# Kernel tuning notes

Hardware: AMD Instinct MI355X
Metric: run time of the kernel (lower is better)

Reference implementation:

```python
import jax, jax.numpy as jnp
import numpy as np

CAP = 15.0
EPS = 1e-6
NUM_HEADS = 16
HEAD_DIM = 64

def _rmsnorm(x, w):
    xf = x.astype(jnp.float32)
    var = jnp.mean(xf * xf, axis=-1, keepdims=True)
    return w * (xf * jax.lax.rsqrt(var + EPS)).astype(x.dtype)

def _gate(g):
    # sigmoid(soft_cap(g)) with cap 15
    return jax.nn.sigmoid(CAP * jnp.tanh(g / CAP))

def setup_inputs() -> dict:
    key = jax.random.key(0)
    ks = jax.random.split(key, 4)
    B, S, D = 4, 2048, 1024
    H, Dh = NUM_HEADS, HEAD_DIM
    return {
        "x": jax.random.normal(ks[0], (B, S, D), jnp.float32),
        "hidden_state": jnp.zeros((B, H, Dh, Dh), jnp.float32),
        "w_rms": jnp.ones((D,), jnp.float32),
        "w_qkv": jax.random.normal(ks[1], (D, 3 * H * Dh), jnp.float32) * 0.02,
        "w_gate": jax.random.normal(ks[2], (D, 3 * H), jnp.float32) * 0.02,
        "w_out": jax.random.normal(ks[3], (D, D), jnp.float32) * 0.02,
    }

def reference(x, hidden_state, w_rms, w_qkv, w_gate, w_out):
    B, S, D = x.shape
    H, Dh = NUM_HEADS, HEAD_DIM
    residual = x
    xn = _rmsnorm(x, w_rms)
    qkv = (xn @ w_qkv).reshape(B, S, 3, H, Dh)
    q, k, v = qkv[:, :, 0], qkv[:, :, 1], qkv[:, :, 2]  # [B,S,H,Dh]
    gates = _gate((xn @ w_gate).reshape(B, S, 3, H))
    i_g, f_g, o_g = gates[:, :, 0], gates[:, :, 1], gates[:, :, 2]  # [B,S,H]

    # time-major for scan: [S,B,H,...]
    def tm(a):
        return jnp.moveaxis(a, 1, 0)

    def step(state, inp):
        qt, kt, vt, it, ft, ot = inp  # [B,H,Dh]/[B,H]
        kv = kt[..., :, None] * vt[..., None, :]            # [B,H,Dh,Dh]
        state = ft[..., None, None] * state + it[..., None, None] * kv
        h = jnp.einsum('bhd,bhde->bhe', qt, state) * ot[..., None]
        return state, h

    _, h_seq = jax.lax.scan(step, hidden_state,
                            (tm(q), tm(k), tm(v), tm(i_g), tm(f_g), tm(o_g)))
    out = jnp.moveaxis(h_seq, 0, 1).reshape(B, S, H * Dh) @ w_out
    return residual + out
```

## Files before the change

### kernel.cpp

```cpp
#include <hip/hip_runtime.h>
#include <math.h>

typedef unsigned short u16;
typedef unsigned int   u32;
typedef __bf16 bf16x8 __attribute__((ext_vector_type(8)));
typedef float  f32x4  __attribute__((ext_vector_type(4)));

#define NBATCH 4
#define SEQ    2048
#define DIM    1024
#define NH     16
#define BH     64
#define NC     32
#define ROWS   8192
#define N1     3328

__device__ __forceinline__ u16 f2bf(float f) {
  u32 u = __builtin_bit_cast(u32, f);
  u32 r = u + 0x7fffu + ((u >> 16) & 1u);
  return (u16)(r >> 16);
}
__device__ __forceinline__ float bf2f(u16 h) {
  return __builtin_bit_cast(float, (u32)h << 16);
}

__device__ __forceinline__ void gl2lds16(const u16* g, u16* l) {
  __builtin_amdgcn_global_load_lds(
      (const __attribute__((address_space(1))) u32*)g,
      (__attribute__((address_space(3))) u32*)l, 16, 0, 0);
}

__global__ __launch_bounds__(256) void transpose_w(const float* __restrict__ W,
                                                   u16* __restrict__ Bt, int K, int N) {
  __shared__ float tile[32][33];
  const int n0 = blockIdx.x * 32, k0 = blockIdx.y * 32;
  const int tx = threadIdx.x, ty = threadIdx.y;
  #pragma unroll
  for (int i = 0; i < 4; i++)
    tile[ty + i * 8][tx] = W[(size_t)(k0 + ty + i * 8) * N + n0 + tx];
  __syncthreads();
  #pragma unroll
  for (int i = 0; i < 4; i++)
    Bt[(size_t)(n0 + ty + i * 8) * K + k0 + tx] = f2bf(tile[tx][ty + i * 8]);
}

__global__ __launch_bounds__(256) void fill_gateW(const float* __restrict__ wg,
                                                  u16* __restrict__ Bt) {
  const int g = blockIdx.x;
  const int tid = threadIdx.x;
  #pragma unroll
  for (int kk = 0; kk < 4; kk++) {
    const int k = kk * 256 + tid;
    u16 v = 0;
    if (g < 48) v = f2bf(wg[(size_t)k * 48 + g]);
    Bt[(size_t)(3072 + g) * 1024 + k] = v;
  }
}

__global__ __launch_bounds__(256) void rmsnorm_k(const float* __restrict__ x,
                                                 const float* __restrict__ w,
                                                 u16* __restrict__ xn) {
  const int row = blockIdx.x, tid = threadIdx.x;
  const float4 xv = *(const float4*)&x[(size_t)row * 1024 + tid * 4];
  float ss = xv.x * xv.x + xv.y * xv.y + xv.z * xv.z + xv.w * xv.w;
  #pragma unroll
  for (int off = 32; off > 0; off >>= 1) ss += __shfl_down(ss, off);
  __shared__ float red[4];
  if ((tid & 63) == 0) red[tid >> 6] = ss;
  __syncthreads();
  const float tot = red[0] + red[1] + red[2] + red[3];
  const float scale = rsqrtf(tot * (1.0f / 1024.0f) + 1e-6f);
  const float4 wv = *(const float4*)&w[tid * 4];
  const u16 o0 = f2bf(xv.x * scale * wv.x), o1 = f2bf(xv.y * scale * wv.y);
  const u16 o2 = f2bf(xv.z * scale * wv.z), o3 = f2bf(xv.w * scale * wv.w);
  uint2 ov;
  ov.x = (u32)o0 | ((u32)o1 << 16);
  ov.y = (u32)o2 | ((u32)o3 << 16);
  *(uint2*)&xn[(size_t)row * 1024 + tid * 4] = ov;
}


#define FENCE asm volatile("" ::: "memory")
#define SBAR  do { FENCE; __builtin_amdgcn_s_barrier(); FENCE; } while (0)
#define WAITV4 do { FENCE; asm volatile("s_waitcnt vmcnt(4)" ::: "memory"); } while (0)
#define WAITV0 do { FENCE; asm volatile("s_waitcnt vmcnt(0)" ::: "memory"); } while (0)

#define STAGE_A(BUF, HALF, TILE) do { \
  const u16* s_ = Abase + (size_t)(TILE) * 64 + (size_t)(HALF) * 131072; \
  u16* l_ = &lds[((BUF) * 4 + (HALF)) * 8192 + tid * 8]; \
  gl2lds16(s_, l_); gl2lds16(s_ + 65536, l_ + 4096); \
} while (0)

#define STAGE_B(BUF, HALF, TILE) do { \
  const u16* s_ = Bbase + (size_t)(TILE) * 64 + (size_t)(HALF) * 131072; \
  u16* l_ = &lds[((BUF) * 4 + 2 + (HALF)) * 8192 + tid * 8]; \
  gl2lds16(s_, l_); gl2lds16(s_ + 65536, l_ + 4096); \
} while (0)

#define READ_A(ALDS, MH) do { \
  _Pragma("unroll") \
  for (int mi_ = 0; mi_ < 4; ++mi_) { \
    af[mi_][0] = *(const bf16x8*)((ALDS) + (MH) * 4096 + mi_ * 1024 + co0); \
    af[mi_][1] = *(const bf16x8*)((ALDS) + (MH) * 4096 + mi_ * 1024 + co1); \
  } \
} while (0)

#define READ_B(BLDS, NH) do { \
  _Pragma("unroll") \
  for (int ni_ = 0; ni_ < 2; ++ni_) { \
    bfr[NH][ni_][0] = *(const bf16x8*)((BLDS) + (NH) * 2048 + ni_ * 1024 + co0); \
    bfr[NH][ni_][1] = *(const bf16x8*)((BLDS) + (NH) * 2048 + ni_ * 1024 + co1); \
  } \
} while (0)

#define MFMA16(MH, NH) do { \
  __builtin_amdgcn_s_setprio(1); \
  _Pragma("unroll") \
  for (int mi_ = 0; mi_ < 4; ++mi_) { \
    _Pragma("unroll") \
    for (int ni_ = 0; ni_ < 2; ++ni_) { \
      acc[(MH)*4+mi_][(NH)*2+ni_] = __builtin_amdgcn_mfma_f32_16x16x32_bf16( \
          af[mi_][0], bfr[NH][ni_][0], acc[(MH)*4+mi_][(NH)*2+ni_], 0, 0, 0); \
      acc[(MH)*4+mi_][(NH)*2+ni_] = __builtin_amdgcn_mfma_f32_16x16x32_bf16( \
          af[mi_][1], bfr[NH][ni_][1], acc[(MH)*4+mi_][(NH)*2+ni_], 0, 0, 0); \
    } \
  } \
  __builtin_amdgcn_s_setprio(0); \
} while (0)

#define GITER(T, FULL) do { \
   READ_A(aLds0, 0); READ_B(bLds0, 0); STAGE_A(1, 0, 2*(T)+1); \
         SBAR; MFMA16(0, 0); SBAR; \
   READ_B(bLds0, 1); STAGE_A(1, 1, 2*(T)+1); \
         SBAR; MFMA16(0, 1); SBAR; \
   READ_A(aLds0, 1); if (FULL) STAGE_B(0, 0, 2*(T)+2); \
         SBAR; MFMA16(1, 0); SBAR; \
   if (FULL) STAGE_B(0, 1, 2*(T)+2); \
         SBAR; MFMA16(1, 1); if (FULL) { WAITV4; } else { WAITV0; } SBAR; \
   READ_A(aLds1, 0); READ_B(bLds1, 0); if (FULL) STAGE_A(0, 0, 2*(T)+2); \
         SBAR; MFMA16(0, 0); SBAR; \
   READ_B(bLds1, 1); if (FULL) STAGE_A(0, 1, 2*(T)+2); \
         SBAR; MFMA16(0, 1); SBAR; \
   READ_A(aLds1, 1); if (FULL) STAGE_B(1, 0, 2*(T)+3); \
         SBAR; MFMA16(1, 0); SBAR; \
   if (FULL) STAGE_B(1, 1, 2*(T)+3); \
         SBAR; MFMA16(1, 1); if (FULL) { WAITV4; } SBAR; \
} while (0)

#define CORE_SETUP(AROWBASE, BCOLBASE) \
  const int tid = threadIdx.x; \
  const int lane = tid & 63, wave = tid >> 6; \
  const int q = lane >> 4, m16 = lane & 15; \
  const int wm = wave & 1, wn = wave >> 1; \
  const int sx = m16 & 7; \
  const int co0 = (q ^ sx) * 8; \
  const int co1 = ((4 + q) ^ sx) * 8; \
  const int r0 = tid >> 3, pc = tid & 7; \
  const int lcg = pc ^ (r0 & 7); \
  const u16* Abase = (AROWBASE) + (size_t)r0 * 1024 + lcg * 8; \
  const u16* Bbase = (BCOLBASE) + (size_t)r0 * 1024 + lcg * 8; \
  const u16* aLds0 = &lds[wm * 8192 + m16 * 64]; \
  const u16* aLds1 = aLds0 + 32768; \
  const u16* bLds0 = &lds[16384 + (wn >> 1) * 8192 + ((wn & 1) * 64 + m16) * 64]; \
  const u16* bLds1 = bLds0 + 32768; \
  bf16x8 af[4][2]; \
  bf16x8 bfr[2][2][2]; \
  f32x4 acc[8][4] = {};

#define CORE_RUN16() do { \
  STAGE_A(0, 0, 0); STAGE_A(0, 1, 0); STAGE_B(0, 0, 0); STAGE_B(0, 1, 0); \
  STAGE_B(1, 0, 1); STAGE_B(1, 1, 1); \
  WAITV4; SBAR; \
  _Pragma("unroll 1") \
  for (int t = 0; t < 7; ++t) GITER(t, 1); \
  GITER(7, 0); \
} while (0)

__global__ __launch_bounds__(512, 2) void gemm_qkv(const u16* __restrict__ A, const u16* __restrict__ Bt,
                                                   u16* __restrict__ Qb, u16* __restrict__ Kb,
                                                   u16* __restrict__ Vb, float* __restrict__ gates) {
  __shared__ __attribute__((aligned(16))) u16 lds[65536];

  const int g = blockIdx.x;
  const int swz = (g & 7) * 52 + (g >> 3);
  const int bm = swz / 13, bn = swz % 13;
  const int rowBase = bm * 256, colBase = bn * 256;

  CORE_SETUP(A + (size_t)rowBase * 1024, Bt + (size_t)colBase * 1024);
  CORE_RUN16();

  const int rr = lane >> 2, co = (lane & 3) * 16;
  if (colBase < 3072) {
    const int which = colBase >> 10;
    u16* dstBase = (which == 0) ? Qb : ((which == 1) ? Kb : Vb);
    const int b = rowBase >> 11;
    const int h = ((colBase & 1023) >> 6) + wn;
    const int tRow0 = (rowBase & 2047) + wm * 128;
    u16* headBase = dstBase + ((size_t)(b * 16 + h)) * 2048 * 64;
    u16* scratch = lds + wave * 1024;
    #pragma unroll
    for (int mi = 0; mi < 8; ++mi) {
      #pragma unroll
      for (int bj = 0; bj < 4; ++bj)
        #pragma unroll
        for (int r = 0; r < 4; ++r)
          scratch[(q * 4 + r) * 64 + bj * 16 + m16] = f2bf(acc[mi][bj][r]);
      const uint4 d0 = *(const uint4*)&scratch[rr * 64 + co];
      const uint4 d1 = *(const uint4*)&scratch[rr * 64 + co + 8];
      u16* gp = headBase + (size_t)(tRow0 + mi * 16 + rr) * 64 + co;
      *(uint4*)gp = d0;
      *(uint4*)(gp + 8) = d1;
    }
  } else {
    if (wn == 0) {
      #pragma unroll
      for (int ai = 0; ai < 8; ++ai)
        #pragma unroll
        for (int bj = 0; bj < 3; ++bj)
          #pragma unroll
          for (int r = 0; r < 4; ++r) {
            const int grow = rowBase + wm * 128 + ai * 16 + q * 4 + r;
            const int b = grow >> 11, tt = grow & 2047;
            const float v = acc[ai][bj][r];
            const float gg = 1.0f / (1.0f + expf(-(15.0f * tanhf(v * (1.0f / 15.0f)))));
            gates[((size_t)bj * 64 + (b * 16 + m16)) * 2048 + tt] = gg;
          }
    }
  }
}

__global__ __launch_bounds__(512, 2) void gemm_out(const u16* __restrict__ A, const u16* __restrict__ Bt,
                                                   const float* __restrict__ resid,
                                                   float* __restrict__ out) {
  __shared__ __attribute__((aligned(16))) u16 lds[65536];

  const int g = blockIdx.x;
  const int swz = (g & 7) * 16 + (g >> 3);
  const int bm = swz >> 2, bn = swz & 3;
  const int rowBase = bm * 256, colBase = bn * 256;

  CORE_SETUP(A + (size_t)rowBase * 1024, Bt + (size_t)colBase * 1024);
  CORE_RUN16();

  const int colW = colBase + (wn >> 1) * 128 + (wn & 1) * 64;
  #pragma unroll
  for (int mi = 0; mi < 8; ++mi)
    #pragma unroll
    for (int bj = 0; bj < 4; ++bj)
      #pragma unroll
      for (int r = 0; r < 4; ++r) {
        const int grow = rowBase + wm * 128 + mi * 16 + q * 4 + r;
        const int gcol = colW + bj * 16 + m16;
        const size_t idx = (size_t)grow * 1024 + gcol;
        out[idx] = acc[mi][bj][r] + resid[idx];
      }
}

__global__ __launch_bounds__(256) void passA_k(const u16* __restrict__ Qb, const u16* __restrict__ Kb,
                                               const u16* __restrict__ Vb,
                                               const float* __restrict__ gates,
                                               float* __restrict__ la,
                                               u16* __restrict__ Mbuf, u16* __restrict__ hseq) {
  __shared__ u16 Ql[64][72], Kl[64][72], KTl[64][72], VTl[64][72], Pl[64][72];
  __shared__ float laS[64], iS[64];
  const int tid = threadIdx.x;
  const int bh = blockIdx.x >> 5, c = blockIdx.x & 31;
  const int lane = tid & 63, w = tid >> 6;
  const int q = lane >> 4, m16 = lane & 15;
  const size_t base = ((size_t)bh * 2048 + c * 64) * 64;
  const int toff = c * 64;

  if (tid < 64) {
    float lg = logf(gates[(size_t)(64 + bh) * 2048 + toff + tid]);
    #pragma unroll
    for (int off = 1; off < 64; off <<= 1) {
      const float y = __shfl_up(lg, off);
      if (tid >= off) lg += y;
    }
    laS[tid] = lg;
    iS[tid] = gates[(size_t)bh * 2048 + toff + tid];
    la[(size_t)bh * 2048 + toff + tid] = lg;
  }
  __syncthreads();

  {
    const int s = tid >> 2, db = (tid & 3) * 16;
    const float wk = expf(laS[63] - laS[s]) * iS[s];
    const uint4 q0 = *(const uint4*)&Qb[base + s * 64 + db];
    const uint4 q1 = *(const uint4*)&Qb[base + s * 64 + db + 8];
    *(uint4*)&Ql[s][db] = q0;
    *(uint4*)&Ql[s][db + 8] = q1;
    const uint4 k0 = *(const uint4*)&Kb[base + s * 64 + db];
    const uint4 k1 = *(const uint4*)&Kb[base + s * 64 + db + 8];
    *(uint4*)&Kl[s][db] = k0;
    *(uint4*)&Kl[s][db + 8] = k1;
    u16 ktmp[16];
    *(uint4*)&ktmp[0] = k0;
    *(uint4*)&ktmp[8] = k1;
    #pragma unroll
    for (int j = 0; j < 16; j++) KTl[db + j][s] = f2bf(wk * bf2f(ktmp[j]));
    const uint4 v0 = *(const uint4*)&Vb[base + s * 64 + db];
    const uint4 v1 = *(const uint4*)&Vb[base + s * 64 + db + 8];
    u16 vtmp[16];
    *(uint4*)&vtmp[0] = v0;
    *(uint4*)&vtmp[8] = v1;
    #pragma unroll
    for (int j = 0; j < 16; j++) VTl[db + j][s] = vtmp[j];
  }
  __syncthreads();

  f32x4 pacc[4] = {};
  #pragma unroll
  for (int ks = 0; ks < 2; ks++) {
    const bf16x8 aq = *(const bf16x8*)&Ql[w * 16 + m16][ks * 32 + q * 8];
    #pragma unroll
    for (int ni = 0; ni < 4; ni++) {
      const bf16x8 bk = *(const bf16x8*)&Kl[ni * 16 + m16][ks * 32 + q * 8];
      pacc[ni] = __builtin_amdgcn_mfma_f32_16x16x32_bf16(aq, bk, pacc[ni], 0, 0, 0);
    }
  }
  #pragma unroll
  for (int ni = 0; ni < 4; ni++)
    #pragma unroll
    for (int r = 0; r < 4; r++) {
      const int tt = w * 16 + q * 4 + r, ss = ni * 16 + m16;
      float Wts = 0.0f;
      if (ss <= tt) Wts = expf(laS[tt] - laS[ss]) * iS[ss];
      Pl[tt][ss] = f2bf(pacc[ni][r] * Wts);
    }
  __syncthreads();

  f32x4 hacc[4] = {}, macc[4] = {};
  #pragma unroll
  for (int ks = 0; ks < 2; ks++) {
    const bf16x8 ap = *(const bf16x8*)&Pl[w * 16 + m16][ks * 32 + q * 8];
    const bf16x8 av = *(const bf16x8*)&VTl[w * 16 + m16][ks * 32 + q * 8];
    #pragma unroll
    for (int ni = 0; ni < 4; ni++) {
      const bf16x8 bv = *(const bf16x8*)&VTl[ni * 16 + m16][ks * 32 + q * 8];
      const bf16x8 bk = *(const bf16x8*)&KTl[ni * 16 + m16][ks * 32 + q * 8];
      hacc[ni] = __builtin_amdgcn_mfma_f32_16x16x32_bf16(ap, bv, hacc[ni], 0, 0, 0);
      macc[ni] = __builtin_amdgcn_mfma_f32_16x16x32_bf16(av, bk, macc[ni], 0, 0, 0);
    }
  }
  const int b = bh >> 4, h = bh & 15;
  #pragma unroll
  for (int ni = 0; ni < 4; ni++)
    #pragma unroll
    for (int r = 0; r < 4; r++) {
      const int tt = w * 16 + q * 4 + r, e = ni * 16 + m16;
      const int tg = c * 64 + tt;
      hseq[((size_t)b * 2048 + tg) * 1024 + h * 64 + e] = f2bf(hacc[ni][r]);
      Mbuf[(((size_t)bh * 32 + c) * 64 + tt) * 64 + e] = f2bf(macc[ni][r]);
    }
}

__global__ __launch_bounds__(256) void passB_k(u16* __restrict__ Mbuf,
                                               const float* __restrict__ hidden,
                                               const float* __restrict__ la) {
  const int bh = blockIdx.x >> 4;
  const int e = (blockIdx.x & 15) * 256 + threadIdx.x;
  __shared__ float Gs[32];
  if (threadIdx.x < 32)
    Gs[threadIdx.x] = expf(la[(size_t)bh * 2048 + threadIdx.x * 64 + 63]);
  __syncthreads();
  const int eRow = e >> 6, dCol = e & 63;
  float st = hidden[(size_t)bh * 4096 + dCol * 64 + eRow];
  u16* M = &Mbuf[(size_t)bh * 32 * 4096 + e];
  float m_next = bf2f(M[0]);
  #pragma unroll 4
  for (int c = 0; c < 32; c++) {
    const float m_cur = m_next;
    if (c < 31) m_next = bf2f(M[(size_t)(c + 1) * 4096]);
    M[(size_t)c * 4096] = f2bf(st);
    st = Gs[c] * st + m_cur;
  }
}

__global__ __launch_bounds__(256) void passC_k(const u16* __restrict__ Qb,
                                               const u16* __restrict__ SprevT,
                                               const float* __restrict__ la,
                                               const float* __restrict__ gates,
                                               u16* __restrict__ hseq) {
  __shared__ u16 aQl[64][72], STl[64][72];
  __shared__ float laS[64], oS[64];
  const int tid = threadIdx.x;
  const int bh = blockIdx.x >> 5, c = blockIdx.x & 31;
  const int lane = tid & 63, w = tid >> 6;
  const int q = lane >> 4, m16 = lane & 15;
  const size_t base = ((size_t)bh * 2048 + c * 64) * 64;
  const int toff = c * 64;
  if (tid < 64) {
    laS[tid] = la[(size_t)bh * 2048 + toff + tid];
    oS[tid] = gates[(size_t)(128 + bh) * 2048 + toff + tid];
  }
  {
    const int s = tid >> 2, db = (tid & 3) * 16;
    *(uint4*)&aQl[s][db]     = *(const uint4*)&Qb[base + s * 64 + db];
    *(uint4*)&aQl[s][db + 8] = *(const uint4*)&Qb[base + s * 64 + db + 8];
    const u16* SpT = &SprevT[((size_t)bh * 32 + c) * 4096];
    *(uint4*)&STl[s][db]     = *(const uint4*)&SpT[s * 64 + db];
    *(uint4*)&STl[s][db + 8] = *(const uint4*)&SpT[s * 64 + db + 8];
  }
  __syncthreads();
  f32x4 acc[4] = {};
  #pragma unroll
  for (int ks = 0; ks < 2; ks++) {
    const bf16x8 a = *(const bf16x8*)&aQl[w * 16 + m16][ks * 32 + q * 8];
    #pragma unroll
    for (int ni = 0; ni < 4; ni++) {
      const bf16x8 bb = *(const bf16x8*)&STl[ni * 16 + m16][ks * 32 + q * 8];
      acc[ni] = __builtin_amdgcn_mfma_f32_16x16x32_bf16(a, bb, acc[ni], 0, 0, 0);
    }
  }
  const int b = bh >> 4, h = bh & 15;
  #pragma unroll
  for (int ni = 0; ni < 4; ni++)
    #pragma unroll
    for (int r = 0; r < 4; r++) {
      const int tt = w * 16 + q * 4 + r, e = ni * 16 + m16;
      const int tg = c * 64 + tt;
      const float a_t = expf(laS[tt]);
      const float o = oS[tt];
      const size_t idx = ((size_t)b * 2048 + tg) * 1024 + h * 64 + e;
      hseq[idx] = f2bf(o * (bf2f(hseq[idx]) + a_t * acc[ni][r]));
    }
}

extern "C" void kernel_launch(void* const* d_in, const int* in_sizes, int n_in,
                              void* d_out, int out_size, void* d_ws, size_t ws_size,
                              hipStream_t stream) {
  (void)in_sizes; (void)n_in; (void)out_size; (void)ws_size;
  const float* x      = (const float*)d_in[0];
  const float* hidden = (const float*)d_in[1];
  const float* w_rms  = (const float*)d_in[2];
  const float* w_qkv  = (const float*)d_in[3];
  const float* w_gate = (const float*)d_in[4];
  const float* w_out  = (const float*)d_in[5];
  float* out = (float*)d_out;

  char* p = (char*)d_ws;
  u16* wqkvT = (u16*)p;  p += (size_t)N1 * 1024 * 2;
  u16* woutT = (u16*)p;  p += (size_t)1024 * 1024 * 2;
  u16* xn    = (u16*)p;  p += (size_t)ROWS * 1024 * 2;
  u16* Qb    = (u16*)p;  p += (size_t)BH * 2048 * 64 * 2;
  u16* Kb    = (u16*)p;  p += (size_t)BH * 2048 * 64 * 2;
  u16* Vb    = (u16*)p;  p += (size_t)BH * 2048 * 64 * 2;
  float* gates = (float*)p; p += (size_t)3 * BH * 2048 * 4;
  float* la    = (float*)p; p += (size_t)BH * 2048 * 4;
  u16* Mbuf  = (u16*)p;  p += (size_t)BH * NC * 4096 * 2;
  u16* hseq  = (u16*)p;  p += (size_t)ROWS * 1024 * 2;

  transpose_w<<<dim3(96, 32), dim3(32, 8), 0, stream>>>(w_qkv, wqkvT, 1024, 3072);
  transpose_w<<<dim3(32, 32), dim3(32, 8), 0, stream>>>(w_out, woutT, 1024, 1024);
  fill_gateW<<<256, 256, 0, stream>>>(w_gate, wqkvT);
  rmsnorm_k<<<ROWS, 256, 0, stream>>>(x, w_rms, xn);
  gemm_qkv<<<416, 512, 0, stream>>>(xn, wqkvT, Qb, Kb, Vb, gates);
  passA_k<<<BH * NC, 256, 0, stream>>>(Qb, Kb, Vb, gates, la, Mbuf, hseq);
  passB_k<<<BH * 16, 256, 0, stream>>>(Mbuf, hidden, la);
  passC_k<<<BH * NC, 256, 0, stream>>>(Qb, Mbuf, la, gates, hseq);
  gemm_out<<<128, 512, 0, stream>>>(hseq, woutT, x, out);
}
```

Measured before the change: 258.6 us.

## Stage chunk outputs through LDS for vector stores, use fast math, reswizzle GEMM tiles

passA and passC now stage their MFMA results in shared memory and write hseq and Mbuf as 16-byte vector stores per row, replacing scattered 2-byte global writes. This is meant to cut uncoalesced global store and read-modify-write traffic. Both GEMMs switch their block-to-tile mapping so consecutive swizzled blocks walk rows first. expf and logf become the __expf and __logf intrinsics, trading a little accuracy in the gates and decay weights for fewer instructions.

```diff
diff --git a/kernel.cpp b/kernel.cpp
--- a/kernel.cpp
+++ b/kernel.cpp
@@ -183,7 +183,7 @@
 
   const int g = blockIdx.x;
   const int swz = (g & 7) * 52 + (g >> 3);
-  const int bm = swz / 13, bn = swz % 13;
+  const int bm = swz & 31, bn = swz >> 5;
   const int rowBase = bm * 256, colBase = bn * 256;
 
   CORE_SETUP(A + (size_t)rowBase * 1024, Bt + (size_t)colBase * 1024);
@@ -222,7 +222,7 @@
             const int grow = rowBase + wm * 128 + ai * 16 + q * 4 + r;
             const int b = grow >> 11, tt = grow & 2047;
             const float v = acc[ai][bj][r];
-            const float gg = 1.0f / (1.0f + expf(-(15.0f * tanhf(v * (1.0f / 15.0f)))));
+            const float gg = 1.0f / (1.0f + __expf(-(15.0f * tanhf(v * (1.0f / 15.0f)))));
             gates[((size_t)bj * 64 + (b * 16 + m16)) * 2048 + tt] = gg;
           }
     }
@@ -236,7 +236,7 @@
 
   const int g = blockIdx.x;
   const int swz = (g & 7) * 16 + (g >> 3);
-  const int bm = swz >> 2, bn = swz & 3;
+  const int bm = swz & 31, bn = swz >> 5;
   const int rowBase = bm * 256, colBase = bn * 256;
 
   CORE_SETUP(A + (size_t)rowBase * 1024, Bt + (size_t)colBase * 1024);
@@ -271,7 +271,7 @@
   const int toff = c * 64;
 
   if (tid < 64) {
-    float lg = logf(gates[(size_t)(64 + bh) * 2048 + toff + tid]);
+    float lg = __logf(gates[(size_t)(64 + bh) * 2048 + toff + tid]);
     #pragma unroll
     for (int off = 1; off < 64; off <<= 1) {
       const float y = __shfl_up(lg, off);
@@ -285,7 +285,7 @@
 
   {
     const int s = tid >> 2, db = (tid & 3) * 16;
-    const float wk = expf(laS[63] - laS[s]) * iS[s];
+    const float wk = __expf(laS[63] - laS[s]) * iS[s];
     const uint4 q0 = *(const uint4*)&Qb[base + s * 64 + db];
     const uint4 q1 = *(const uint4*)&Qb[base + s * 64 + db + 8];
     *(uint4*)&Ql[s][db] = q0;
@@ -325,7 +325,7 @@
     for (int r = 0; r < 4; r++) {
       const int tt = w * 16 + q * 4 + r, ss = ni * 16 + m16;
       float Wts = 0.0f;
-      if (ss <= tt) Wts = expf(laS[tt] - laS[ss]) * iS[ss];
+      if (ss <= tt) Wts = __expf(laS[tt] - laS[ss]) * iS[ss];
       Pl[tt][ss] = f2bf(pacc[ni][r] * Wts);
     }
   __syncthreads();
@@ -343,16 +343,27 @@
       macc[ni] = __builtin_amdgcn_mfma_f32_16x16x32_bf16(av, bk, macc[ni], 0, 0, 0);
     }
   }
-  const int b = bh >> 4, h = bh & 15;
+
+  __syncthreads();
   #pragma unroll
   for (int ni = 0; ni < 4; ni++)
     #pragma unroll
     for (int r = 0; r < 4; r++) {
       const int tt = w * 16 + q * 4 + r, e = ni * 16 + m16;
-      const int tg = c * 64 + tt;
-      hseq[((size_t)b * 2048 + tg) * 1024 + h * 64 + e] = f2bf(hacc[ni][r]);
-      Mbuf[(((size_t)bh * 32 + c) * 64 + tt) * 64 + e] = f2bf(macc[ni][r]);
-    }
+      Pl[tt][e] = f2bf(hacc[ni][r]);
+      Kl[tt][e] = f2bf(macc[ni][r]);
+    }
+  __syncthreads();
+  {
+    const int s = tid >> 2, db = (tid & 3) * 16;
+    const int b = bh >> 4, h = bh & 15;
+    u16* hp = &hseq[((size_t)b * 2048 + c * 64 + s) * 1024 + h * 64 + db];
+    *(uint4*)hp       = *(const uint4*)&Pl[s][db];
+    *(uint4*)(hp + 8) = *(const uint4*)&Pl[s][db + 8];
+    u16* mp = &Mbuf[(((size_t)bh * 32 + c) * 64 + s) * 64 + db];
+    *(uint4*)mp       = *(const uint4*)&Kl[s][db];
+    *(uint4*)(mp + 8) = *(const uint4*)&Kl[s][db + 8];
+  }
 }
 
 __global__ __launch_bounds__(256) void passB_k(u16* __restrict__ Mbuf,
@@ -362,7 +373,7 @@
   const int e = (blockIdx.x & 15) * 256 + threadIdx.x;
   __shared__ float Gs[32];
   if (threadIdx.x < 32)
-    Gs[threadIdx.x] = expf(la[(size_t)bh * 2048 + threadIdx.x * 64 + 63]);
+    Gs[threadIdx.x] = __expf(la[(size_t)bh * 2048 + threadIdx.x * 64 + 63]);
   __syncthreads();
   const int eRow = e >> 6, dCol = e & 63;
   float st = hidden[(size_t)bh * 4096 + dCol * 64 + eRow];
@@ -383,6 +394,7 @@
                                                const float* __restrict__ gates,
                                                u16* __restrict__ hseq) {
   __shared__ u16 aQl[64][72], STl[64][72];
+  __shared__ float hstage[64][68];
   __shared__ float laS[64], oS[64];
   const int tid = threadIdx.x;
   const int bh = blockIdx.x >> 5, c = blockIdx.x & 31;
@@ -413,18 +425,34 @@
       acc[ni] = __builtin_amdgcn_mfma_f32_16x16x32_bf16(a, bb, acc[ni], 0, 0, 0);
     }
   }
-  const int b = bh >> 4, h = bh & 15;
   #pragma unroll
   for (int ni = 0; ni < 4; ni++)
     #pragma unroll
-    for (int r = 0; r < 4; r++) {
-      const int tt = w * 16 + q * 4 + r, e = ni * 16 + m16;
-      const int tg = c * 64 + tt;
-      const float a_t = expf(laS[tt]);
-      const float o = oS[tt];
-      const size_t idx = ((size_t)b * 2048 + tg) * 1024 + h * 64 + e;
-      hseq[idx] = f2bf(o * (bf2f(hseq[idx]) + a_t * acc[ni][r]));
-    }
+    for (int r = 0; r < 4; r++)
+      hstage[w * 16 + q * 4 + r][ni * 16 + m16] = acc[ni][r];
+  __syncthreads();
+  {
+    const int s = tid >> 2, db = (tid & 3) * 16;
+    const int b = bh >> 4, h = bh & 15;
+    const float a_t = __expf(laS[s]);
+    const float o = oS[s];
+    u16* hp = &hseq[((size_t)b * 2048 + c * 64 + s) * 1024 + h * 64 + db];
+    uint4 h0 = *(const uint4*)hp, h1 = *(const uint4*)(hp + 8);
+    u16 hv[16];
+    *(uint4*)&hv[0] = h0;
+    *(uint4*)&hv[8] = h1;
+    float sv[16];
+    *(float4*)&sv[0]  = *(const float4*)&hstage[s][db];
+    *(float4*)&sv[4]  = *(const float4*)&hstage[s][db + 4];
+    *(float4*)&sv[8]  = *(const float4*)&hstage[s][db + 8];
+    *(float4*)&sv[12] = *(const float4*)&hstage[s][db + 12];
+    u16 ov[16];
+    #pragma unroll
+    for (int j = 0; j < 16; j++)
+      ov[j] = f2bf(o * (bf2f(hv[j]) + a_t * sv[j]));
+    *(uint4*)hp       = *(const uint4*)&ov[0];
+    *(uint4*)(hp + 8) = *(const uint4*)&ov[8];
+  }
 }
 
 extern "C" void kernel_launch(void* const* d_in, const int* in_sizes, int n_in,
```

Result: no change. 259.6 us (+0.4%).
